# Kernel tuning notes

Hardware: AMD Instinct MI355X
Metric: run time of the kernel (lower is better)

Reference implementation:

```python
import jax, jax.numpy as jnp
import numpy as np

N, T, V, C, O = 64, 512, 17, 3, 64
EPS = 1e-5  # torch BatchNorm eps


def _bn(x, gamma, beta):
    # training-mode BatchNorm2d over (N, H, W) per channel, biased variance
    m = jnp.mean(x, axis=(0, 2, 3), keepdims=True)
    v = jnp.var(x, axis=(0, 2, 3), keepdims=True)
    return gamma.reshape(1, -1, 1, 1) * (x - m) * jax.lax.rsqrt(v + EPS) + beta.reshape(1, -1, 1, 1)


def setup_inputs() -> dict:
    key = jax.random.key(0)
    ks = jax.random.split(key, 20)
    f32 = jnp.float32
    PA = (jnp.eye(V, dtype=f32) / (1.0 + 1e-5))  # row-normalized identity, as in reset_parameter
    return {
        "x": jax.random.normal(ks[0], (N, T, V, C), f32),
        "w1": jax.random.normal(ks[1], (C, C), f32) * 0.5,
        "b1": jax.random.normal(ks[2], (C,), f32) * 0.1,
        "w2": jax.random.normal(ks[3], (C, C), f32) * 0.5,
        "b2": jax.random.normal(ks[4], (C,), f32) * 0.1,
        "convT_w": jax.random.normal(ks[5], (C,), f32) * 0.5,      # Conv2d(3,1,1) weight squeezed
        "convT_b": jax.random.normal(ks[6], (), f32) * 0.1,
        "convT_gamma": jnp.ones((), f32),
        "convT_beta": jnp.zeros((), f32),
        "PA": PA,
        "alpha": jnp.ones((V, V), f32),
        "conv2d_w": jax.random.normal(ks[7], (O, C), f32) * (2.0 / (O * 1 * 1)) ** 0.5,  # conv_branch_init
        "conv2d_b": jnp.zeros((O,), f32),
        "bn_gamma": jnp.full((O,), 1e-6, f32),  # bn_init(self.bn, 1e-6)
        "bn_beta": jnp.zeros((O,), f32),
        "pool_w": jax.random.normal(ks[8], (O, C), f32) * (2.0 / C) ** 0.5,  # kaiming fan_out-ish
        "pool_b": jnp.zeros((O,), f32),
        "pool_gamma": jnp.ones((O,), f32),
        "pool_beta": jnp.zeros((O,), f32),
    }


def reference(x, w1, b1, w2, b2, convT_w, convT_b, convT_gamma, convT_beta,
              PA, alpha, conv2d_w, conv2d_b, bn_gamma, bn_beta,
              pool_w, pool_b, pool_gamma, pool_beta):
    # x: (N, T, V, C)
    x1 = x @ w1.T + b1                     # linear1, (N,T,V,C)
    x2 = x @ w2.T + b2                     # linear2
    # d[n,t,i,j,c] = x1[n,t,j,c] - x2[n,t,i,c]; the 1x1 conv over C is linear,
    # so contract with convT_w BEFORE broadcasting to avoid the (N,T,V,V,C) tensor.
    a1 = x1 @ convT_w                      # (N,T,V)
    a2 = x2 @ convT_w                      # (N,T,V)
    s = a1[:, :, None, :] - a2[:, :, :, None] + convT_b   # (N,T,V,V)
    # BatchNorm2d(1): single channel -> stats over the whole tensor; then ReLU
    m = jnp.mean(s)
    var = jnp.var(s)
    s = jax.nn.relu(convT_gamma * (s - m) * jax.lax.rsqrt(var + EPS) + convT_beta)
    # temporal abs-diff, sum over T, mean over batch -> learned adjacency offset (V,V)
    a3 = jnp.mean(jnp.sum(jnp.abs(s[:, 1:] - s[:, :-1]), axis=1), axis=0)
    # NOTE: the original does x.view(N, C, T, V) -- a raw memory reinterpretation,
    # NOT a permute. Replicate with reshape.
    xr = x.reshape(N, C, T, V)
    A = PA + alpha * a3                    # (V,V)
    y = (xr.reshape(N, C * T, V) @ A).reshape(N, C, T, V)
    z = jnp.einsum('nctv,oc->notv', y, conv2d_w) + conv2d_b[None, :, None, None]
    z = _bn(z, bn_gamma, bn_beta)
    p = jnp.einsum('nctv,oc->notv', xr, pool_w) + pool_b[None, :, None, None]
    p = _bn(p, pool_gamma, pool_beta)
    out = jax.nn.relu(z + p)               # (N,O,T,V)
    return out.reshape(N, T, V, O)         # raw reshape, matching torch .reshape
```

## Files before the change

### kernel.cpp

```cpp
#include <hip/hip_runtime.h>

constexpr int Nn = 64, Tt = 512, Vv = 17, Oo = 64;
constexpr int TV  = Tt * Vv;
constexpr int CTV = 3 * TV;
constexpr float EPSf = 1e-5f;
constexpr int NG   = 51;
constexpr int GSTR = 2688;
constexpr int NGE  = 2652;
constexpr int BTV  = 1088;

__device__ inline int div17(int v) { return (int)(((unsigned)v * 61681u) >> 20); }
__device__ inline int div272(int v) { return (int)(((unsigned)v * 15421u) >> 22); }

__device__ inline double wred(double v) {
#pragma unroll
  for (int o = 32; o > 0; o >>= 1) v += __shfl_down(v, o, 64);
  return v;
}

__global__ void __launch_bounds__(256) k1(
    const float* __restrict__ x,
    const float* __restrict__ w1, const float* __restrict__ b1,
    const float* __restrict__ w2, const float* __restrict__ b2,
    const float* __restrict__ cw, const float* __restrict__ cb,
    double* __restrict__ spart, float* __restrict__ gpart)
{
  __shared__ float wr[64 * 56];
  __shared__ float xsA[64 * 51];
  __shared__ double dred[4][5];
  const int tid = threadIdx.x, bid = blockIdx.x;
  const int n = bid >> 3, ch = bid & 7;
  {
    const float4* src = (const float4*)(x + (size_t)bid * 3264);
    float4* dst = (float4*)xsA;
    for (int i = tid; i < 816; i += 256) dst[i] = src[i];
  }
#pragma unroll
  for (int c = 0; c < 3; ++c) {
    const float4* src = (const float4*)(x + (size_t)n * CTV + (size_t)c * TV + ch * BTV);
    for (int i = tid; i < 272; i += 256) {
      float4 v = src[i];
      int p = i * 4;
      float vv[4] = { v.x, v.y, v.z, v.w };
#pragma unroll
      for (int k = 0; k < 4; ++k) {
        int pp = p + k; int t = div17(pp), u = pp - t * 17;
        wr[t * 56 + c * 17 + u] = vv[k];
      }
    }
  }
  for (int i = tid; i < 64 * 5; i += 256) { int t = i / 5, j = 51 + (i - t * 5); wr[t * 56 + j] = 0.f; }
  __syncthreads();
  float u1[3], u2[3];
#pragma unroll
  for (int k = 0; k < 3; ++k) {
    float s1 = 0.f, s2 = 0.f;
#pragma unroll
    for (int c = 0; c < 3; ++c) { s1 += cw[c] * w1[c * 3 + k]; s2 += cw[c] * w2[c * 3 + k]; }
    u1[k] = s1; u2[k] = s2;
  }
  float d1 = 0.f, d2 = 0.f;
#pragma unroll
  for (int c = 0; c < 3; ++c) { d1 += b1[c] * cw[c]; d2 += b2[c] * cw[c]; }
  const float bb = cb[0];
  if (tid < 49) {
    const int r8 = (tid / 7) * 8, c8 = (tid - (tid / 7) * 7) * 8;
    float acc[8][8];
#pragma unroll
    for (int a = 0; a < 8; ++a)
#pragma unroll
      for (int b = 0; b < 8; ++b) acc[a][b] = 0.f;
    for (int t = 0; t < 64; ++t) {
      const float* row = &wr[t * 56];
      float4 ra0 = *(const float4*)(row + r8), ra1 = *(const float4*)(row + r8 + 4);
      float4 cb0 = *(const float4*)(row + c8), cb1 = *(const float4*)(row + c8 + 4);
      float ae[8] = { ra0.x, ra0.y, ra0.z, ra0.w, ra1.x, ra1.y, ra1.z, ra1.w };
      float be[8] = { cb0.x, cb0.y, cb0.z, cb0.w, cb1.x, cb1.y, cb1.z, cb1.w };
#pragma unroll
      for (int a = 0; a < 8; ++a)
#pragma unroll
        for (int b = 0; b < 8; ++b) acc[a][b] = fmaf(ae[a], be[b], acc[a][b]);
    }
    float* gp = gpart + (size_t)bid * GSTR;
#pragma unroll
    for (int a = 0; a < 8; ++a) {
      int j = r8 + a;
      if (j < NG) {
#pragma unroll
        for (int b = 0; b < 8; ++b) {
          int jp = c8 + b;
          if (jp < NG) gp[j * NG + jp] = acc[a][b];
        }
      }
    }
  }
  double st[5] = {0, 0, 0, 0, 0};
  if (tid >= 64 && tid < 128) {
    const float* rp = &xsA[(tid - 64) * 51];
    float A = 0.f, G = 0.f, Q1 = 0.f, Q2 = 0.f;
#pragma unroll
    for (int v = 0; v < 17; ++v) {
      float x0 = rp[v * 3], x1 = rp[v * 3 + 1], x2 = rp[v * 3 + 2];
      float va1 = fmaf(x0, u1[0], fmaf(x1, u1[1], fmaf(x2, u1[2], d1)));
      float va2 = fmaf(x0, u2[0], fmaf(x1, u2[1], fmaf(x2, u2[2], d2)));
      float g = bb - va2;
      A += va1; G += g;
      Q1 = fmaf(va1, va1, Q1); Q2 = fmaf(g, g, Q2);
    }
    st[0] = A; st[1] = G; st[2] = Q1; st[3] = Q2; st[4] = (double)A * (double)G;
  }
  if (tid >= 128 && tid < 128 + NG) {
    int j = tid - 128;
    float m = 0.f;
    for (int t = 0; t < 64; ++t) m += wr[t * 56 + j];
    gpart[(size_t)bid * GSTR + NG * NG + j] = m;
  }
  {
    int wv = tid >> 6;
#pragma unroll
    for (int s = 0; s < 5; ++s) { double r = wred(st[s]); if ((tid & 63) == 0) dred[wv][s] = r; }
  }
  __syncthreads();
  if (tid < 5)
    spart[(size_t)bid * 5 + tid] = dred[0][tid] + dred[1][tid] + dred[2][tid] + dred[3][tid];
}

__global__ void __launch_bounds__(256) k2(
    const float* __restrict__ x, const double* __restrict__ spart,
    const float* __restrict__ gpart,
    const float* __restrict__ w1, const float* __restrict__ b1,
    const float* __restrict__ w2, const float* __restrict__ b2,
    const float* __restrict__ cw, const float* __restrict__ cb,
    const float* __restrict__ cg_, const float* __restrict__ cbeta,
    float* __restrict__ a3part, double* __restrict__ gramF)
{
  __shared__ float l1t[17 * 260];
  __shared__ float l2t[17 * 260];
  __shared__ float segsum[289 * 4];
  __shared__ double dred[4][21];
  __shared__ float sfl[2];
  const int tid = threadIdx.x;
  const int h = blockIdx.x, n = blockIdx.y;
  const int jb = n * 2 + h;
  const int t0 = h * 256;
  const int wv = tid >> 6;
  {
    double v5[5];
#pragma unroll
    for (int s = 0; s < 5; ++s)
      v5[s] = spart[(size_t)tid * 5 + s] + spart[(size_t)(tid + 256) * 5 + s];
#pragma unroll
    for (int s = 0; s < 5; ++s) { double r = wred(v5[s]); if ((tid & 63) == 0) dred[wv][s] = r; }
  }
  __syncthreads();
  if (tid == 0) {
    double S[5];
#pragma unroll
    for (int s = 0; s < 5; ++s) S[s] = dred[0][s] + dred[1][s] + dred[2][s] + dred[3][s];
    double cnt = (double)Nn * Tt * Vv * Vv;
    double mean = ((double)Vv * (S[0] + S[1])) / cnt;
    double m2   = ((double)Vv * (S[2] + S[3]) + 2.0 * S[4]) / cnt;
    double var  = m2 - mean * mean;
    double scale = (double)cg_[0] / sqrt(var + (double)EPSf);
    double shift = (double)cbeta[0] + scale * ((double)cb[0] - mean);
    sfl[0] = (float)scale; sfl[1] = (float)(shift - scale * (double)cb[0]);
  }
  __syncthreads();
  {
    int e0 = jb * 21;
    double gv[21];
    const float* g1 = gpart + (size_t)tid * GSTR + e0;
    const float* g2 = gpart + (size_t)(tid + 256) * GSTR + e0;
#pragma unroll
    for (int k = 0; k < 21; ++k) gv[k] = (double)g1[k] + (double)g2[k];
#pragma unroll
    for (int k = 0; k < 21; ++k) { double r = wred(gv[k]); if ((tid & 63) == 0) dred[wv][k] = r; }
    __syncthreads();
    if (tid < 21 && e0 + tid < NGE)
      gramF[e0 + tid] = dred[0][tid] + dred[1][tid] + dred[2][tid] + dred[3][tid];
  }
  float u1[3], u2[3];
#pragma unroll
  for (int k = 0; k < 3; ++k) {
    float s1 = 0.f, s2 = 0.f;
#pragma unroll
    for (int c = 0; c < 3; ++c) { s1 += cw[c] * w1[c * 3 + k]; s2 += cw[c] * w2[c * 3 + k]; }
    u1[k] = s1; u2[k] = s2;
  }
  float d1 = 0.f, d2 = 0.f;
#pragma unroll
  for (int c = 0; c < 3; ++c) { d1 += b1[c] * cw[c]; d2 += b2[c] * cw[c]; }
  const float bb = cb[0];
  const int nst = (h == 0) ? 257 : 256;
  const float* xb = x + ((size_t)(n * Tt + t0)) * 51;
  for (int idx = tid; idx < nst * 17; idx += 256) {
    int r = div17(idx), v = idx - r * 17;
    const float* xp = xb + idx * 3;
    float x0 = xp[0], x1 = xp[1], x2 = xp[2];
    float va1 = fmaf(x0, u1[0], fmaf(x1, u1[1], fmaf(x2, u1[2], d1)));
    float va2 = fmaf(x0, u2[0], fmaf(x1, u2[1], fmaf(x2, u2[2], d2)));
    l1t[v * 260 + r] = va1; l2t[v * 260 + r] = bb - va2;
  }
  __syncthreads();
  {
    const float scale = sfl[0], c0 = sfl[1];
    for (int task = tid; task < 289 * 4; task += 256) {
      int e = task >> 2, s = task & 3;
      int i = div17(e), j = e - i * 17;
      int ts = s * 64;
      bool hasb = !(h == 1 && s == 3);
      const float* J = &l1t[j * 260];
      const float* I = &l2t[i * 260];
      float prev = fmaxf(fmaf(scale, J[ts] + I[ts], c0), 0.f);
      float acc = 0.f;
#pragma unroll 4
      for (int q = 0; q < 16; ++q) {
        float4 a4 = *(const float4*)(J + ts + q * 4);
        float4 b4 = *(const float4*)(I + ts + q * 4);
        float z0 = fmaxf(fmaf(scale, a4.x + b4.x, c0), 0.f);
        float z1 = fmaxf(fmaf(scale, a4.y + b4.y, c0), 0.f);
        float z2 = fmaxf(fmaf(scale, a4.z + b4.z, c0), 0.f);
        float z3 = fmaxf(fmaf(scale, a4.w + b4.w, c0), 0.f);
        if (q > 0) acc += fabsf(z0 - prev);
        acc += fabsf(z1 - z0) + fabsf(z2 - z1) + fabsf(z3 - z2);
        prev = z3;
      }
      if (hasb) {
        float zb = fmaxf(fmaf(scale, J[ts + 64] + I[ts + 64], c0), 0.f);
        acc += fabsf(zb - prev);
      }
      segsum[e * 4 + s] = acc;
    }
  }
  __syncthreads();
  for (int e = tid; e < 289; e += 256) {
    float s = (segsum[e * 4] + segsum[e * 4 + 1]) + (segsum[e * 4 + 2] + segsum[e * 4 + 3]);
    a3part[(size_t)jb * 289 + e] = s;
  }
}

__global__ void __launch_bounds__(256, 2) k3(
    const float* __restrict__ x,
    const float* __restrict__ PA, const float* __restrict__ alpha,
    const float* __restrict__ a3part, const double* __restrict__ gramF,
    const float* __restrict__ c2w, const float* __restrict__ c2b,
    const float* __restrict__ bng, const float* __restrict__ bnb,
    const float* __restrict__ pw, const float* __restrict__ pb,
    const float* __restrict__ pg, const float* __restrict__ pbeta,
    float* __restrict__ out)
{
  __shared__ float xs[3 * BTV], ys[3 * BTV];
  __shared__ float As[289], Bh[289], rsA[17], coefs[512];
  __shared__ double mom[18];
  const int tid = threadIdx.x, bid = blockIdx.x;
  const int n = bid >> 3, ch = bid & 7;
  const int t0c = ch * BTV;

#pragma unroll
  for (int c = 0; c < 3; ++c) {
    const float4* src = (const float4*)(x + (size_t)n * CTV + (size_t)c * TV + t0c);
    float4* dst = (float4*)(xs + c * BTV);
    for (int i = tid; i < 272; i += 256) dst[i] = src[i];
  }

  for (int e = tid; e < 289; e += 256) {
    float acc = 0.f;
#pragma unroll 4
    for (int j = 0; j < 128; ++j) acc += a3part[(size_t)j * 289 + e];
    As[e] = fmaf(alpha[e], acc * (1.0f / Nn), PA[e]);
  }
  __syncthreads();

  for (int k = tid; k < 289; k += 256) {
    int u = div17(k), up = k - u * 17;
    float s = 0.f;
#pragma unroll
    for (int v = 0; v < 17; ++v) s = fmaf(As[u * 17 + v], As[up * 17 + v], s);
    Bh[k] = s;
  }
  if (tid < 17) {
    float s = 0.f;
#pragma unroll
    for (int v = 0; v < 17; ++v) s += As[tid * 17 + v];
    rsA[tid] = s;
  }
  __syncthreads();

  {
    const int pc0[6] = {0, 0, 0, 1, 1, 2};
    const int pc1[6] = {0, 1, 2, 1, 2, 2};
    if (tid < 192) {
      int p = tid >> 5, r = tid & 31;
      int c = pc0[p], cp = pc1[p];
      double s = 0.0;
      for (int k = r; k < 289; k += 32) {
        int u = div17(k), up = k - u * 17;
        s += gramF[(c * 17 + u) * NG + cp * 17 + up] * (double)Bh[k];
      }
#pragma unroll
      for (int off = 16; off > 0; off >>= 1) s += __shfl_down(s, off, 32);
      if (r == 0) mom[3 + p] = s;
    } else if (tid < 198) {
      int p = tid - 192; const int c = pc0[p], cp = pc1[p];
      double s = 0.0;
#pragma unroll
      for (int u = 0; u < 17; ++u) s += gramF[(c * 17 + u) * NG + cp * 17 + u];
      mom[12 + p] = s;
    } else if (tid < 201) {
      int c = tid - 198; double s = 0.0;
#pragma unroll
      for (int u = 0; u < 17; ++u) s += gramF[NG * NG + c * 17 + u] * (double)rsA[u];
      mom[c] = s;
    } else if (tid < 204) {
      int c = tid - 201; double s = 0.0;
#pragma unroll
      for (int u = 0; u < 17; ++u) s += gramF[NG * NG + c * 17 + u];
      mom[9 + c] = s;
    }
  }
  __syncthreads();

  if (tid < 64) {
    int o = tid;
    const double cnt = (double)Nn * Tt * Vv;
    double my0 = mom[0] / cnt, my1 = mom[1] / cnt, my2 = mom[2] / cnt;
    double e00 = mom[3] / cnt, e01 = mom[4] / cnt, e02 = mom[5] / cnt;
    double e11 = mom[6] / cnt, e12 = mom[7] / cnt, e22 = mom[8] / cnt;
    double mx0 = mom[9] / cnt, mx1 = mom[10] / cnt, mx2 = mom[11] / cnt;
    double f00 = mom[12] / cnt, f01 = mom[13] / cnt, f02 = mom[14] / cnt;
    double f11 = mom[15] / cnt, f12 = mom[16] / cnt, f22 = mom[17] / cnt;
    double w0 = c2w[o * 3], w1_ = c2w[o * 3 + 1], w2_ = c2w[o * 3 + 2], bz = c2b[o];
    double wm = w0 * my0 + w1_ * my1 + w2_ * my2, mz = wm + bz;
    double Ez2 = w0 * w0 * e00 + 2 * w0 * w1_ * e01 + 2 * w0 * w2_ * e02
               + w1_ * w1_ * e11 + 2 * w1_ * w2_ * e12 + w2_ * w2_ * e22
               + 2 * bz * wm + bz * bz;
    double sz = (double)bng[o] / sqrt(Ez2 - mz * mz + (double)EPSf);
    double q0 = pw[o * 3], q1 = pw[o * 3 + 1], q2 = pw[o * 3 + 2], bp = pb[o];
    double qm = q0 * mx0 + q1 * mx1 + q2 * mx2, mp = qm + bp;
    double Ep2 = q0 * q0 * f00 + 2 * q0 * q1 * f01 + 2 * q0 * q2 * f02
               + q1 * q1 * f11 + 2 * q1 * q2 * f12 + q2 * q2 * f22
               + 2 * bp * qm + bp * bp;
    double sp = (double)pg[o] / sqrt(Ep2 - mp * mp + (double)EPSf);
    coefs[o * 8 + 0] = (float)(sz * w0); coefs[o * 8 + 1] = (float)(sz * w1_); coefs[o * 8 + 2] = (float)(sz * w2_);
    coefs[o * 8 + 3] = (float)(sp * q0); coefs[o * 8 + 4] = (float)(sp * q1); coefs[o * 8 + 5] = (float)(sp * q2);
    coefs[o * 8 + 6] = (float)(sz * (bz - mz) + (double)bnb[o] + sp * (bp - mp) + (double)pbeta[o]);
    coefs[o * 8 + 7] = 0.f;
  }
#pragma unroll
  for (int k = 0; k < 5; ++k) {
    int e = k * 256 + tid;
    if (e < BTV) {
      int tr = div17(e), v = e - tr * 17;
      float y0 = 0.f, y1 = 0.f, y2 = 0.f;
#pragma unroll
      for (int u = 0; u < 17; ++u) {
        float a = As[u * 17 + v];
        y0 = fmaf(xs[tr * 17 + u], a, y0);
        y1 = fmaf(xs[BTV + tr * 17 + u], a, y1);
        y2 = fmaf(xs[2 * BTV + tr * 17 + u], a, y2);
      }
      ys[e] = y0; ys[BTV + e] = y1; ys[2 * BTV + e] = y2;
    }
  }
  __syncthreads();

  float* obase = out + (size_t)n * ((size_t)Oo * TV) + t0c;
#pragma unroll 2
  for (int g = 0; g < 17; ++g) {
    int base = g * 256 + tid;
    int o0 = div272(base);
    int tq = (base - o0 * 272) * 4;
    float4 y0 = *(const float4*)&ys[tq];
    float4 y1 = *(const float4*)&ys[BTV + tq];
    float4 y2 = *(const float4*)&ys[2 * BTV + tq];
    float4 x0 = *(const float4*)&xs[tq];
    float4 x1 = *(const float4*)&xs[BTV + tq];
    float4 x2 = *(const float4*)&xs[2 * BTV + tq];
    float* ob = obase + (size_t)o0 * TV + tq;
#pragma unroll
    for (int j = 0; j < 4; ++j) {
      int o = o0 + (j << 4);
      float4 ca = *(const float4*)&coefs[o * 8];
      float4 cv = *(const float4*)&coefs[o * 8 + 4];
      float4 r;
      r.x = fmaxf(fmaf(ca.x, y0.x, fmaf(ca.y, y1.x, fmaf(ca.z, y2.x,
            fmaf(ca.w, x0.x, fmaf(cv.x, x1.x, fmaf(cv.y, x2.x, cv.z)))))), 0.f);
      r.y = fmaxf(fmaf(ca.x, y0.y, fmaf(ca.y, y1.y, fmaf(ca.z, y2.y,
            fmaf(ca.w, x0.y, fmaf(cv.x, x1.y, fmaf(cv.y, x2.y, cv.z)))))), 0.f);
      r.z = fmaxf(fmaf(ca.x, y0.z, fmaf(ca.y, y1.z, fmaf(ca.z, y2.z,
            fmaf(ca.w, x0.z, fmaf(cv.x, x1.z, fmaf(cv.y, x2.z, cv.z)))))), 0.f);
      r.w = fmaxf(fmaf(ca.x, y0.w, fmaf(ca.y, y1.w, fmaf(ca.z, y2.w,
            fmaf(ca.w, x0.w, fmaf(cv.x, x1.w, fmaf(cv.y, x2.w, cv.z)))))), 0.f);
      *(float4*)(ob + (size_t)(j << 4) * TV) = r;
    }
  }
}

extern "C" void kernel_launch(void* const* d_in, const int* in_sizes, int n_in,
                              void* d_out, int out_size, void* d_ws, size_t ws_size,
                              hipStream_t stream)
{
  (void)in_sizes; (void)n_in; (void)out_size; (void)ws_size;
  const float* x     = (const float*)d_in[0];
  const float* w1    = (const float*)d_in[1];
  const float* b1    = (const float*)d_in[2];
  const float* w2    = (const float*)d_in[3];
  const float* b2    = (const float*)d_in[4];
  const float* cw    = (const float*)d_in[5];
  const float* cb    = (const float*)d_in[6];
  const float* cg_   = (const float*)d_in[7];
  const float* cbeta = (const float*)d_in[8];
  const float* PA    = (const float*)d_in[9];
  const float* alpha = (const float*)d_in[10];
  const float* c2w   = (const float*)d_in[11];
  const float* c2b   = (const float*)d_in[12];
  const float* bng   = (const float*)d_in[13];
  const float* bnb   = (const float*)d_in[14];
  const float* pw    = (const float*)d_in[15];
  const float* pb    = (const float*)d_in[16];
  const float* pg    = (const float*)d_in[17];
  const float* pbeta = (const float*)d_in[18];
  float* out = (float*)d_out;

  char* ws = (char*)d_ws;
  double* spart  = (double*)(ws + 0);
  float*  gpart  = (float*)(ws + 20480);
  float*  a3part = (float*)(ws + 5525504);
  double* gramF  = (double*)(ws + 5673472);

  hipLaunchKernelGGL(k1, dim3(512), dim3(256), 0, stream,
                     x, w1, b1, w2, b2, cw, cb, spart, gpart);
  hipLaunchKernelGGL(k2, dim3(2, Nn), dim3(256), 0, stream,
                     x, spart, gpart, w1, b1, w2, b2, cw, cb, cg_, cbeta, a3part, gramF);
  hipLaunchKernelGGL(k3, dim3(512), dim3(256), 0, stream,
                     x, PA, alpha, a3part, gramF, c2w, c2b, bng, bnb,
                     pw, pb, pg, pbeta, out);
}
```

Measured before the change: 87.86 us.

## Split k1 Gram accumulation across four waves and widen a3part reduction ILP

In k1 the 51x51 Gram product, previously computed by only 49 threads of the first wave over all 64 time rows, is now split so each of the four waves handles 16 rows. The partial results go to shared memory and are summed before a coalesced write to global memory. The per-row stats work moves to wave 0. In k3 the 128-way a3part reduction uses four independent accumulators to raise memory-level parallelism. The cost is about 41KB of extra shared memory per block, which may lower occupancy, plus an extra barrier and changed float summation order.

```diff
diff --git a/kernel.cpp b/kernel.cpp
--- a/kernel.cpp
+++ b/kernel.cpp
@@ -27,9 +27,12 @@
 {
   __shared__ float wr[64 * 56];
   __shared__ float xsA[64 * 51];
+  __shared__ float gpw[4][2601];
   __shared__ double dred[4][5];
   const int tid = threadIdx.x, bid = blockIdx.x;
   const int n = bid >> 3, ch = bid & 7;
+  const int wv = tid >> 6, lane = tid & 63;
+
   {
     const float4* src = (const float4*)(x + (size_t)bid * 3264);
     float4* dst = (float4*)xsA;
@@ -51,6 +54,7 @@
   }
   for (int i = tid; i < 64 * 5; i += 256) { int t = i / 5, j = 51 + (i - t * 5); wr[t * 56 + j] = 0.f; }
   __syncthreads();
+
   float u1[3], u2[3];
 #pragma unroll
   for (int k = 0; k < 3; ++k) {
@@ -63,14 +67,16 @@
 #pragma unroll
   for (int c = 0; c < 3; ++c) { d1 += b1[c] * cw[c]; d2 += b2[c] * cw[c]; }
   const float bb = cb[0];
-  if (tid < 49) {
-    const int r8 = (tid / 7) * 8, c8 = (tid - (tid / 7) * 7) * 8;
+
+  if (lane < 49) {
+    const int r8 = (lane / 7) * 8, c8 = (lane - (lane / 7) * 7) * 8;
+    const int tbeg = wv * 16;
     float acc[8][8];
 #pragma unroll
     for (int a = 0; a < 8; ++a)
 #pragma unroll
       for (int b = 0; b < 8; ++b) acc[a][b] = 0.f;
-    for (int t = 0; t < 64; ++t) {
+    for (int t = tbeg; t < tbeg + 16; ++t) {
       const float* row = &wr[t * 56];
       float4 ra0 = *(const float4*)(row + r8), ra1 = *(const float4*)(row + r8 + 4);
       float4 cb0 = *(const float4*)(row + c8), cb1 = *(const float4*)(row + c8 + 4);
@@ -81,7 +87,7 @@
 #pragma unroll
         for (int b = 0; b < 8; ++b) acc[a][b] = fmaf(ae[a], be[b], acc[a][b]);
     }
-    float* gp = gpart + (size_t)bid * GSTR;
+    float* gw = gpw[wv];
 #pragma unroll
     for (int a = 0; a < 8; ++a) {
       int j = r8 + a;
@@ -89,14 +95,27 @@
 #pragma unroll
         for (int b = 0; b < 8; ++b) {
           int jp = c8 + b;
-          if (jp < NG) gp[j * NG + jp] = acc[a][b];
+          if (jp < NG) gw[j * NG + jp] = acc[a][b];
         }
       }
     }
   }
+  __syncthreads();
+
+  {
+    float* gp = gpart + (size_t)bid * GSTR;
+    for (int e = tid; e < NG * NG; e += 256)
+      gp[e] = (gpw[0][e] + gpw[1][e]) + (gpw[2][e] + gpw[3][e]);
+  }
+  if (tid >= 128 && tid < 128 + NG) {
+    int j = tid - 128;
+    float m = 0.f;
+    for (int t = 0; t < 64; ++t) m += wr[t * 56 + j];
+    gpart[(size_t)bid * GSTR + NG * NG + j] = m;
+  }
   double st[5] = {0, 0, 0, 0, 0};
-  if (tid >= 64 && tid < 128) {
-    const float* rp = &xsA[(tid - 64) * 51];
+  if (tid < 64) {
+    const float* rp = &xsA[tid * 51];
     float A = 0.f, G = 0.f, Q1 = 0.f, Q2 = 0.f;
 #pragma unroll
     for (int v = 0; v < 17; ++v) {
@@ -109,17 +128,8 @@
     }
     st[0] = A; st[1] = G; st[2] = Q1; st[3] = Q2; st[4] = (double)A * (double)G;
   }
-  if (tid >= 128 && tid < 128 + NG) {
-    int j = tid - 128;
-    float m = 0.f;
-    for (int t = 0; t < 64; ++t) m += wr[t * 56 + j];
-    gpart[(size_t)bid * GSTR + NG * NG + j] = m;
-  }
-  {
-    int wv = tid >> 6;
-#pragma unroll
-    for (int s = 0; s < 5; ++s) { double r = wred(st[s]); if ((tid & 63) == 0) dred[wv][s] = r; }
-  }
+#pragma unroll
+  for (int s = 0; s < 5; ++s) { double r = wred(st[s]); if (lane == 0) dred[wv][s] = r; }
   __syncthreads();
   if (tid < 5)
     spart[(size_t)bid * 5 + tid] = dred[0][tid] + dred[1][tid] + dred[2][tid] + dred[3][tid];
@@ -264,9 +274,16 @@
   }
 
   for (int e = tid; e < 289; e += 256) {
-    float acc = 0.f;
-#pragma unroll 4
-    for (int j = 0; j < 128; ++j) acc += a3part[(size_t)j * 289 + e];
+    const float* p = a3part + e;
+    float a0 = 0.f, a1 = 0.f, a2 = 0.f, a3 = 0.f;
+#pragma unroll 8
+    for (int j = 0; j < 128; j += 4) {
+      a0 += p[(size_t)(j + 0) * 289];
+      a1 += p[(size_t)(j + 1) * 289];
+      a2 += p[(size_t)(j + 2) * 289];
+      a3 += p[(size_t)(j + 3) * 289];
+    }
+    float acc = (a0 + a1) + (a2 + a3);
     As[e] = fmaf(alpha[e], acc * (1.0f / Nn), PA[e]);
   }
   __syncthreads();
```

Measured after the change: 82.90 us. 1.06x faster.
